# Optimization experiments

Hardware: AMD Instinct MI355X
Metric: run time of the kernel (lower is better)

The kernel has to match this reference:

```python
import jax, jax.numpy as jnp
import numpy as np
from jax import lax

FEAT_STRIDE = 16
PRE_NMS_TOP_N = 6000   # cfg['TEST'].RPN_PRE_NMS_TOP_N
POST_NMS_TOP_N = 300   # cfg['TEST'].RPN_POST_NMS_TOP_N
NMS_THRESH = 0.7       # cfg['TEST'].RPN_NMS_THRESH
MIN_SIZE = 16.0        # cfg['TEST'].RPN_MIN_SIZE
B, A, H, W = 32, 9, 128, 128
NEG_INF = jnp.float32(-1e30)


def _whctrs(a):
    w = a[2] - a[0] + 1.0
    h = a[3] - a[1] + 1.0
    return w, h, a[0] + 0.5 * (w - 1), a[1] + 0.5 * (h - 1)

def _mkanchors(ws, hs, xc, yc):
    ws = ws[:, None]; hs = hs[:, None]
    return np.hstack((xc - 0.5 * (ws - 1), yc - 0.5 * (hs - 1),
                      xc + 0.5 * (ws - 1), yc + 0.5 * (hs - 1)))

def _ratio_enum(anchor, ratios):
    w, h, xc, yc = _whctrs(anchor)
    size = w * h
    ws = np.round(np.sqrt(size / ratios))
    hs = np.round(ws * ratios)
    return _mkanchors(ws, hs, xc, yc)

def _scale_enum(anchor, scales):
    w, h, xc, yc = _whctrs(anchor)
    return _mkanchors(w * scales, h * scales, xc, yc)

def generate_anchors(base_size=16, ratios=np.array([0.5, 1.0, 2.0]), scales=np.array([8.0, 16.0, 32.0])):
    base = np.array([1, 1, base_size, base_size], dtype=np.float64) - 1
    ra = _ratio_enum(base, ratios)
    return np.vstack([_scale_enum(ra[i], scales) for i in range(ra.shape[0])]).astype(np.float32)

_BASE_ANCHORS = generate_anchors()  # (A, 4)

def _all_anchors(h, w):
    sx = np.arange(w) * FEAT_STRIDE
    sy = np.arange(h) * FEAT_STRIDE
    sx, sy = np.meshgrid(sx, sy)  # row-major (h, w) matches permute(0,2,3,1) ordering
    shifts = np.stack([sx.ravel(), sy.ravel(), sx.ravel(), sy.ravel()], axis=1).astype(np.float32)
    return jnp.asarray((shifts[:, None, :] + _BASE_ANCHORS[None, :, :]).reshape(-1, 4))  # (h*w*A, 4)

# ---- bbox_transform_inv / clip_boxes ----

def _decode(anchors, deltas):
    ws = anchors[:, 2] - anchors[:, 0] + 1.0
    hs = anchors[:, 3] - anchors[:, 1] + 1.0
    cx = anchors[:, 0] + 0.5 * ws
    cy = anchors[:, 1] + 0.5 * hs
    dx, dy, dw, dh = deltas[:, 0], deltas[:, 1], deltas[:, 2], deltas[:, 3]
    pcx = dx * ws + cx
    pcy = dy * hs + cy
    pw = jnp.exp(dw) * ws
    ph = jnp.exp(dh) * hs
    return jnp.stack([pcx - 0.5 * pw, pcy - 0.5 * ph, pcx + 0.5 * pw, pcy + 0.5 * ph], axis=1)

def _clip(b, imh, imw):
    x1 = jnp.clip(b[:, 0], 0.0, imw - 1.0)
    y1 = jnp.clip(b[:, 1], 0.0, imh - 1.0)
    x2 = jnp.clip(b[:, 2], 0.0, imw - 1.0)
    y2 = jnp.clip(b[:, 3], 0.0, imh - 1.0)
    return jnp.stack([x1, y1, x2, y2], axis=1)

# ---- greedy NMS: pick top-score box, suppress IoU > thresh, repeat POST times ----

def _nms_select(boxes, scores):
    # boxes: (PRE, 4) score-sorted; scores: (PRE,)
    areas = (boxes[:, 2] - boxes[:, 0] + 1.0) * (boxes[:, 3] - boxes[:, 1] + 1.0)

    def body(i, st):
        s, keep, valid = st
        j = jnp.argmax(s)
        keep = keep.at[i].set(j)
        valid = valid.at[i].set(s[j] > NEG_INF)
        b = boxes[j]
        xx1 = jnp.maximum(b[0], boxes[:, 0])
        yy1 = jnp.maximum(b[1], boxes[:, 1])
        xx2 = jnp.minimum(b[2], boxes[:, 2])
        yy2 = jnp.minimum(b[3], boxes[:, 3])
        inter = jnp.maximum(xx2 - xx1 + 1.0, 0.0) * jnp.maximum(yy2 - yy1 + 1.0, 0.0)
        iou = inter / jnp.maximum(areas[j] + areas - inter, 1e-6)
        s = jnp.where(iou > NMS_THRESH, NEG_INF, s)  # suppresses j itself (IoU = 1)
        return s, keep, valid

    init = (scores, jnp.zeros((POST_NMS_TOP_N,), jnp.int32), jnp.zeros((POST_NMS_TOP_N,), bool))
    _, keep, valid = lax.fori_loop(0, POST_NMS_TOP_N, body, init)
    return keep, valid

def _per_image(sc, dl, info, anchors):
    prop = _clip(_decode(anchors, dl), info[0], info[1])  # (K*A, 4)
    ws = prop[:, 2] - prop[:, 0] + 1.0
    hs = prop[:, 3] - prop[:, 1] + 1.0
    min_sz = MIN_SIZE * info[2]
    sc = jnp.where((ws >= min_sz) & (hs >= min_sz), sc, NEG_INF)
    top_s, top_i = lax.top_k(sc, PRE_NMS_TOP_N)
    cand = prop[top_i]  # (PRE, 4)
    keep, valid = _nms_select(cand, top_s)
    return cand[keep] * valid[:, None].astype(cand.dtype)  # zero-pad invalid rows

def _forward(rpn_cls_prob, rpn_bbox_pred, im_info):
    b, _, h, w = rpn_cls_prob.shape
    anchors = _all_anchors(h, w)
    scores = rpn_cls_prob[:, A:, :, :].transpose(0, 2, 3, 1).reshape(b, -1)  # (b, h*w*A)
    deltas = rpn_bbox_pred.transpose(0, 2, 3, 1).reshape(b, -1, 4)           # (b, h*w*A, 4)
    boxes = jax.vmap(lambda s, d, i: _per_image(s, d, i, anchors))(scores, deltas, im_info)
    ids = jnp.broadcast_to(jnp.arange(b, dtype=boxes.dtype)[:, None, None], (b, POST_NMS_TOP_N, 1))
    return jnp.concatenate([ids, boxes], axis=2)  # (b, POST, 5): [batch_idx, x1, y1, x2, y2]

def setup_inputs() -> dict:
    key = jax.random.key(0)
    k1, k2 = jax.random.split(key)
    rpn_cls_prob = jax.random.uniform(k1, (B, 2 * A, H, W), dtype=jnp.float32)
    rpn_bbox_pred = jax.random.normal(k2, (B, 4 * A, H, W), dtype=jnp.float32) * 0.2
    im_info = jnp.tile(jnp.array([[H * FEAT_STRIDE, W * FEAT_STRIDE, 1.0]], dtype=jnp.float32), (B, 1))
    return {"rpn_cls_prob": rpn_cls_prob, "rpn_bbox_pred": rpn_bbox_pred, "im_info": im_info}

def reference(rpn_cls_prob, rpn_bbox_pred, im_info):
    return _forward(rpn_cls_prob, rpn_bbox_pred, im_info)
```

## Files before the change

kernel.cpp:

```cpp
#include <hip/hip_runtime.h>
#include <cstdint>
#include <cstddef>

#pragma clang fp contract(off)

typedef unsigned long long u64;

#define NB 32
#define NA 9
#define NH 128
#define NW 128
#define HW (NH*NW)
#define NANCH (NA*HW)
#define PRE_N 6000
#define POST_N 300
#define CAND_CAP 8192
#define NMS_T 0.7f
#define GX_GATHER 24
#define NBOX 6144
#define CH 512

__constant__ float c_wa[9] = {184.f,368.f,736.f,128.f,256.f,512.f,88.f,176.f,352.f};
__constant__ float c_ha[9] = {96.f,192.f,384.f,128.f,256.f,512.f,176.f,352.f,704.f};

__device__ __forceinline__ float4 decode_clip(int a, int h, int w,
    float dx, float dy, float dlw, float dlh, float imh, float imw) {
  float wa = c_wa[a], ha = c_ha[a];
  float cx = (float)w * 16.0f + 8.0f;
  float cy = (float)h * 16.0f + 8.0f;
  float pcx = dx * wa + cx;
  float pcy = dy * ha + cy;
  float pw = expf(dlw) * wa;
  float ph = expf(dlh) * ha;
  float x1 = pcx - 0.5f * pw;
  float y1 = pcy - 0.5f * ph;
  float x2 = pcx + 0.5f * pw;
  float y2 = pcy + 0.5f * ph;
  float4 r;
  r.x = fminf(fmaxf(x1, 0.0f), imw - 1.0f);
  r.y = fminf(fmaxf(y1, 0.0f), imh - 1.0f);
  r.z = fminf(fmaxf(x2, 0.0f), imw - 1.0f);
  r.w = fminf(fmaxf(y2, 0.0f), imh - 1.0f);
  return r;
}

__device__ __forceinline__ unsigned score_key(float sc, float bw, float bh, float msz) {
  unsigned bits = __float_as_uint(sc);
  unsigned key = (bits & 0x80000000u) ? ~bits : (bits | 0x80000000u);
  if (!(bw >= msz && bh >= msz)) key = 0u;
  return key;
}

__device__ __forceinline__ bool sup_test4(float4 v, float ar, float4 p, float pa) {
  float xx1 = fmaxf(p.x, v.x), yy1 = fmaxf(p.y, v.y);
  float xx2 = fminf(p.z, v.z), yy2 = fminf(p.w, v.w);
  float iw = fmaxf(xx2 - xx1 + 1.0f, 0.0f);
  float ih = fmaxf(yy2 - yy1 + 1.0f, 0.0f);
  float inter = iw * ih;
  float iou = inter / fmaxf(pa + ar - inter, 1e-6f);
  return iou > NMS_T;
}

__device__ __forceinline__ u64 shfl_xor_u64(u64 x, int m) {
  int lo = __shfl_xor((int)(unsigned)x, m, 64);
  int hi = __shfl_xor((int)(unsigned)(x >> 32), m, 64);
  return ((u64)(unsigned)hi << 32) | (unsigned)lo;
}

__device__ __forceinline__ void reg_step(u64 v[8], int t, int k, int j) {
  #pragma unroll
  for (int r = 0; r < 8; ++r) {
    if ((r & j) == 0) {
      int e = (t << 3) + r;
      bool up = ((e & k) == 0);
      u64 x = v[r], y = v[r | j];
      u64 mx = x > y ? x : y, mn = x > y ? y : x;
      v[r]     = up ? mx : mn;
      v[r | j] = up ? mn : mx;
    }
  }
}

__device__ __forceinline__ void shfl_step(u64 v[8], int t, int k, int j) {
  int m = j >> 3;
  bool lower = ((t & m) == 0);
  #pragma unroll
  for (int r = 0; r < 8; ++r) {
    int e = (t << 3) + r;
    bool up = ((e & k) == 0);
    u64 pv = shfl_xor_u64(v[r], m);
    bool keepmax = (up == lower);
    u64 x = v[r];
    u64 mx = x > pv ? x : pv, mn = x > pv ? pv : x;
    v[r] = keepmax ? mx : mn;
  }
}

__device__ __forceinline__ void lds_step(u64* sm, u64 v[8], int t, int k, int j) {
  int m = j >> 3;
  __syncthreads();
  #pragma unroll
  for (int r = 0; r < 8; ++r) sm[(r << 10) | t] = v[r];
  __syncthreads();
  bool lower = ((t & m) == 0);
  bool up = (((t << 3) & k) == 0);
  bool keepmax = (up == lower);
  int pt = t ^ m;
  #pragma unroll
  for (int r = 0; r < 8; ++r) {
    u64 pv = sm[(r << 10) | pt];
    u64 x = v[r];
    u64 mx = x > pv ? x : pv, mn = x > pv ? pv : x;
    v[r] = keepmax ? mx : mn;
  }
}

__device__ void find_B(const unsigned* __restrict__ hb, unsigned* part,
                       unsigned* outB, unsigned* outCum) {
  int tid = threadIdx.x;
  unsigned s = 0;
  for (int i = 0; i < 16; ++i) s += hb[tid*16 + i];
  part[tid] = s;
  __syncthreads();
  for (int off = 1; off < 256; off <<= 1) {
    unsigned v = (tid + off < 256) ? part[tid + off] : 0u;
    __syncthreads();
    part[tid] += v;
    __syncthreads();
  }
  unsigned St = part[tid];
  unsigned Sn = (tid < 255) ? part[tid + 1] : 0u;
  if (St >= (unsigned)PRE_N && Sn < (unsigned)PRE_N) {
    unsigned cum = Sn, B = 0, cumAbove = Sn;
    for (int i = 15; i >= 0; --i) {
      unsigned v = hb[tid*16 + i];
      if (cum + v >= (unsigned)PRE_N) { B = (unsigned)(tid*16 + i); cumAbove = cum; break; }
      cum += v;
    }
    *outB = B; *outCum = cumAbove;
  }
  __syncthreads();
}

__device__ void find_thr(const unsigned* __restrict__ hb2, unsigned B, unsigned cum0,
                         unsigned* part, unsigned* outThr) {
  int tid = threadIdx.x;
  unsigned s = 0;
  for (int i = 0; i < 16; ++i) s += hb2[tid*16 + i];
  part[tid] = s;
  __syncthreads();
  for (int off = 1; off < 256; off <<= 1) {
    unsigned v = (tid + off < 256) ? part[tid + off] : 0u;
    __syncthreads();
    part[tid] += v;
    __syncthreads();
  }
  unsigned St = cum0 + part[tid];
  unsigned Sn = cum0 + ((tid < 255) ? part[tid + 1] : 0u);
  if (St >= (unsigned)PRE_N && Sn < (unsigned)PRE_N) {
    unsigned cum = Sn, t = 1u;
    for (int i = 15; i >= 0; --i) {
      unsigned v = hb2[tid*16 + i];
      if (cum + v >= (unsigned)PRE_N) {
        t = (B << 20) | ((unsigned)(tid*16 + i) << 8);
        break;
      }
      cum += v;
    }
    if (t == 0u) t = 1u;
    *outThr = t;
  }
  __syncthreads();
}

__global__ __launch_bounds__(256) void k_keys(const float* __restrict__ cls,
    const float* __restrict__ dl, const float* __restrict__ info,
    unsigned* __restrict__ keys, unsigned* __restrict__ hist) {
  __shared__ unsigned hsh[4096];
  int tid = threadIdx.x;
  for (int i = tid; i < 4096; i += 256) hsh[i] = 0;
  int t = blockIdx.x * 256 + tid;
  int b = blockIdx.y;
  int hw0 = t * 4;
  int h = hw0 >> 7;
  const float* dlb  = dl  + (size_t)b * (4*NA*HW);
  const float* clsb = cls + (size_t)b * (2*NA*HW);
  float imh = info[b*3+0], imw = info[b*3+1];
  float msz = 16.0f * info[b*3+2];
  unsigned* kb = keys + (size_t)b * NANCH;
  __syncthreads();
  #pragma unroll
  for (int a = 0; a < 9; ++a) {
    float4 dx4 = *(const float4*)&dlb[(a*4+0)*HW + hw0];
    float4 dy4 = *(const float4*)&dlb[(a*4+1)*HW + hw0];
    float4 dw4 = *(const float4*)&dlb[(a*4+2)*HW + hw0];
    float4 dh4 = *(const float4*)&dlb[(a*4+3)*HW + hw0];
    float4 sc4 = *(const float4*)&clsb[(NA+a)*HW + hw0];
    uint4 out;
    {
      float4 bx = decode_clip(a, h, (hw0+0)&127, dx4.x, dy4.x, dw4.x, dh4.x, imh, imw);
      out.x = score_key(sc4.x, bx.z-bx.x+1.0f, bx.w-bx.y+1.0f, msz);
    }
    {
      float4 bx = decode_clip(a, h, (hw0+1)&127, dx4.y, dy4.y, dw4.y, dh4.y, imh, imw);
      out.y = score_key(sc4.y, bx.z-bx.x+1.0f, bx.w-bx.y+1.0f, msz);
    }
    {
      float4 bx = decode_clip(a, h, (hw0+2)&127, dx4.z, dy4.z, dw4.z, dh4.z, imh, imw);
      out.z = score_key(sc4.z, bx.z-bx.x+1.0f, bx.w-bx.y+1.0f, msz);
    }
    {
      float4 bx = decode_clip(a, h, (hw0+3)&127, dx4.w, dy4.w, dw4.w, dh4.w, imh, imw);
      out.w = score_key(sc4.w, bx.z-bx.x+1.0f, bx.w-bx.y+1.0f, msz);
    }
    *(uint4*)&kb[a*HW + hw0] = out;
    atomicAdd(&hsh[out.x >> 20], 1u);
    atomicAdd(&hsh[out.y >> 20], 1u);
    atomicAdd(&hsh[out.z >> 20], 1u);
    atomicAdd(&hsh[out.w >> 20], 1u);
  }
  __syncthreads();
  unsigned* gb = hist + ((size_t)b << 12);
  for (int i = tid; i < 4096; i += 256) {
    unsigned v = hsh[i];
    if (v) atomicAdd(&gb[i], v);
  }
}

__global__ __launch_bounds__(256) void k_hist2(const unsigned* __restrict__ keys,
    const unsigned* __restrict__ hist1, unsigned* __restrict__ hist2) {
  __shared__ unsigned h[4096];
  __shared__ unsigned part[256];
  __shared__ unsigned sB, sCum;
  int b = blockIdx.y, tid = threadIdx.x;
  for (int i = tid; i < 4096; i += 256) h[i] = 0;
  __syncthreads();
  find_B(hist1 + ((size_t)b << 12), part, &sB, &sCum);
  unsigned B = sB;
  const unsigned* kb = keys + (size_t)b * NANCH;
  for (int i = blockIdx.x * 256 + tid; i < NANCH; i += gridDim.x * 256) {
    unsigned k = kb[i];
    if ((k >> 20) == B) atomicAdd(&h[(k >> 8) & 4095u], 1u);
  }
  __syncthreads();
  unsigned* gb = hist2 + ((size_t)b << 12);
  for (int i = tid; i < 4096; i += 256) { unsigned v = h[i]; if (v) atomicAdd(&gb[i], v); }
}

__global__ __launch_bounds__(256) void k_gather(const unsigned* __restrict__ keys,
    const unsigned* __restrict__ hist1, const unsigned* __restrict__ hist2,
    const float* __restrict__ dl, const float* __restrict__ info,
    unsigned* __restrict__ cnt, u64* __restrict__ cand,
    float4* __restrict__ boxes) {
  int b = blockIdx.y, tid = threadIdx.x;
  int lane = tid & 63, wv = tid >> 6;
  __shared__ unsigned part[256];
  __shared__ unsigned sB, sCum, sThr;
  __shared__ unsigned wcnt[4], woff[4], blkbase;
  if (tid == 0) sThr = 1u;
  __syncthreads();
  find_B(hist1 + ((size_t)b << 12), part, &sB, &sCum);
  find_thr(hist2 + ((size_t)b << 12), sB, sCum, part, &sThr);
  unsigned t_ = sThr;
  const unsigned* kb = keys + (size_t)b * NANCH;
  const float* dlb = dl + (size_t)b * (4*NA*HW);
  float imh = info[b*3+0], imw = info[b*3+1];
  u64* cb = cand + (size_t)b * CAND_CAP;
  float4* bxc = boxes + (size_t)b * CAND_CAP;
  unsigned* cp = cnt + (size_t)b * 64;
  const int PER_BLK = NANCH / GX_GATHER;
  int base0 = blockIdx.x * PER_BLK;
  for (int it = 0; it < PER_BLK / 256; ++it) {
    int j = base0 + it * 256 + tid;
    unsigned key = kb[j];
    bool pass = key >= t_;
    u64 mask = __ballot(pass);
    if (lane == 0) wcnt[wv] = (unsigned)__popcll(mask);
    __syncthreads();
    if (tid == 0) {
      unsigned s0 = 0;
      for (int w = 0; w < 4; ++w) { woff[w] = s0; s0 += wcnt[w]; }
      blkbase = s0 ? atomicAdd(cp, s0) : 0u;
    }
    __syncthreads();
    if (pass) {
      unsigned pos = blkbase + woff[wv] + (unsigned)__popcll(mask & ((1ull << lane) - 1ull));
      if (pos < CAND_CAP) {
        int a = j >> 14, hw = j & (HW - 1);
        unsigned oi = (unsigned)(hw * 9 + a);
        unsigned noi = (~oi) & 0x3FFFFu;
        cb[pos] = ((u64)key << 32) | ((u64)noi << 13) | (u64)pos;
        bxc[pos] = decode_clip(a, hw >> 7, hw & 127,
                               dlb[(a*4+0)*HW + hw], dlb[(a*4+1)*HW + hw],
                               dlb[(a*4+2)*HW + hw], dlb[(a*4+3)*HW + hw],
                               imh, imw);
      }
    }
    __syncthreads();
  }
}

__global__ __launch_bounds__(1024) void k_final4(const u64* __restrict__ cand,
    const unsigned* __restrict__ cnt, const float4* __restrict__ boxes,
    float* __restrict__ out) {
  __shared__ float4 bx[NBOX];
  __shared__ float4 cbox2[CH];
  __shared__ float  carea2[CH];
  __shared__ float4 kbox[POST_N];
  __shared__ float  karea[POST_N];
  __shared__ unsigned supf[CH];
  __shared__ u64 sup[CH][9];
  __shared__ u64 aliveM[8];
  __shared__ u64 kgW[8];
  __shared__ int s_nk;
  u64* sm = (u64*)bx;

  int b = blockIdx.x, tid = threadIdx.x;
  int lane = tid & 63;
  if (tid == 0) s_nk = 0;

  unsigned effcnt = cnt[b * 64];
  if (effcnt > CAND_CAP) effcnt = CAND_CAP;
  const u64* cb = cand + (size_t)b * CAND_CAP;
  int e0 = tid << 3;
  u64 v[8];
  #pragma unroll
  for (int r = 0; r < 8; ++r)
    v[r] = ((unsigned)(e0 + r) < effcnt) ? cb[e0 + r] : 0ull;

  for (int k = 2; k <= 8; k <<= 1)
    for (int j = k >> 1; j >= 1; j >>= 1) reg_step(v, tid, k, j);
  for (int k = 16; k <= CAND_CAP; k <<= 1) {
    int j = k >> 1;
    for (; j >= 512; j >>= 1) lds_step(sm, v, tid, k, j);
    for (; j >= 8;   j >>= 1) shfl_step(v, tid, k, j);
    for (; j >= 1;   j >>= 1) reg_step(v, tid, k, j);
  }
  __syncthreads();

  const float4* bxc = boxes + (size_t)b * CAND_CAP;
  #pragma unroll
  for (int r = 0; r < 8; ++r) {
    int rank = e0 + r;
    if (rank < NBOX) {
      u64 ck = (rank < PRE_N) ? v[r] : 0ull;
      float4 w = make_float4(0.f, 0.f, -1.f, -1.f);
      if ((unsigned)(ck >> 32) != 0u)
        w = bxc[(unsigned)(ck & 0x1FFFu)];
      bx[rank] = w;
    }
  }
  __syncthreads();

  float* ob = out + (size_t)b * (POST_N * 5);
  int c = tid & (CH - 1);
  int seg = tid >> 9;

  for (int base = 0; base < NBOX; base += CH) {
    if (tid < CH) {
      float4 w = bx[base + tid];
      supf[tid] = (w.z - w.x + 1.0f > 0.0f) ? 0u : 1u;
    }
    __syncthreads();
    int nk0 = s_nk;

    if (supf[c] == 0u && nk0 > 0) {
      float4 w = bx[base + c];
      float ar = (w.z - w.x + 1.0f) * (w.w - w.y + 1.0f);
      bool dead = false;
      for (int k = seg; k < nk0; k += 2) {
        if (sup_test4(w, ar, kbox[k], karea[k])) { dead = true; break; }
      }
      if (dead) supf[c] = 1u;
    }
    __syncthreads();

    if (tid < CH) {
      u64 am = __ballot(supf[tid] == 0u);
      if (lane == 0) aliveM[tid >> 6] = am;
    }
    __syncthreads();

    int na = 0;
    #pragma unroll
    for (int g = 0; g < 8; ++g) na += (int)__popcll(aliveM[g]);
    if (na == 0) continue;

    if (tid < CH && supf[tid] == 0u) {
      int cg2 = tid >> 6;
      int pre = 0;
      #pragma unroll
      for (int g = 0; g < 8; ++g) if (g < cg2) pre += (int)__popcll(aliveM[g]);
      pre += (int)__popcll(aliveM[cg2] & ((1ull << (tid & 63)) - 1ull));
      float4 w = bx[base + tid];
      cbox2[pre] = w;
      carea2[pre] = (w.z - w.x + 1.0f) * (w.w - w.y + 1.0f);
    }
    __syncthreads();

    {
      int i = c;
      if (i < na) {
        int ngi = (i >> 6) + 1;
        int gA = seg ? (ngi >> 1) : 0;
        int gB = seg ? ngi : (ngi >> 1);
        if (gA < gB) {
          float4 vi = cbox2[i];
          float ai = carea2[i];
          for (int g = gA; g < gB; ++g) {
            int jmax = i - (g << 6);
            if (jmax > 64) jmax = 64;
            u64 r = 0;
            #pragma unroll 4
            for (int j = 0; j < jmax; ++j) {
              if (sup_test4(vi, ai, cbox2[(g << 6) + j], carea2[(g << 6) + j]))
                r |= 1ull << j;
            }
            sup[i][g] = r;
          }
        }
      }
    }
    __syncthreads();

    if (tid < 64) {
      u64 kw[8];
      #pragma unroll
      for (int s = 0; s < 8; ++s) {
        u64 kg = 0;
        if (s * 64 < na) {
          int cc = s * 64 + lane;
          bool a = (cc < na);
          #pragma unroll
          for (int g = 0; g < 8; ++g) {
            if (g < s && a) a = (sup[cc][g] & kw[g]) == 0ull;
          }
          u64 r = a ? sup[cc][s] : 0ull;
          u64 cm = __ballot(a);
          while (cm) {
            int j = __builtin_ctzll(cm);
            kg |= 1ull << j;
            u64 rem = __ballot((r >> j) & 1ull);
            cm &= ~(rem | (1ull << j));
          }
        }
        kw[s] = kg;
      }
      if (lane == 0) {
        #pragma unroll
        for (int s = 0; s < 8; ++s) kgW[s] = kw[s];
      }
    }
    __syncthreads();

    if (tid < na) {
      int s = tid >> 6;
      u64 kgw = kgW[s];
      bool kept = (kgw >> (tid & 63)) & 1;
      int pre = 0;
      #pragma unroll
      for (int g = 0; g < 8; ++g) if (g < s) pre += (int)__popcll(kgW[g]);
      pre += (int)__popcll(kgw & ((1ull << (tid & 63)) - 1ull));
      int rank = nk0 + pre;
      if (kept && rank < POST_N) {
        float4 w = cbox2[tid];
        kbox[rank] = w; karea[rank] = carea2[tid];
        ob[rank*5+0] = (float)b;
        ob[rank*5+1] = w.x; ob[rank*5+2] = w.y; ob[rank*5+3] = w.z; ob[rank*5+4] = w.w;
      }
    }
    if (tid == 0) {
      int tot = 0;
      #pragma unroll
      for (int s = 0; s < 8; ++s) tot += (int)__popcll(kgW[s]);
      int nn = nk0 + tot;
      s_nk = nn < POST_N ? nn : POST_N;
    }
    __syncthreads();
    if (s_nk >= POST_N) break;
  }
  __syncthreads();
  int nk = s_nk;
  for (int r = nk + tid; r < POST_N; r += 1024) {
    ob[r*5+0] = (float)b;
    ob[r*5+1] = 0.f; ob[r*5+2] = 0.f; ob[r*5+3] = 0.f; ob[r*5+4] = 0.f;
  }
}

extern "C" void kernel_launch(void* const* d_in, const int* in_sizes, int n_in,
                              void* d_out, int out_size, void* d_ws, size_t ws_size,
                              hipStream_t stream) {
  const float* cls  = (const float*)d_in[0];
  const float* dl   = (const float*)d_in[1];
  const float* info = (const float*)d_in[2];
  float* out = (float*)d_out;
  char* ws = (char*)d_ws;

  const size_t OFF_KEYS = 0;
  const size_t OFF_H1   = 18874368;
  const size_t OFF_H2   = 19398656;
  const size_t OFF_CNT  = 19922944;
  const size_t OFF_CAND = 19931136;
  const size_t OFF_BOX  = 22028288;
  const size_t WS_NEED  = 26222592;
  if (ws_size < WS_NEED) return;

  unsigned* keys  = (unsigned*)(ws + OFF_KEYS);
  unsigned* h1    = (unsigned*)(ws + OFF_H1);
  unsigned* h2    = (unsigned*)(ws + OFF_H2);
  unsigned* cnt   = (unsigned*)(ws + OFF_CNT);
  u64* cand = (u64*)(ws + OFF_CAND);
  float4* boxes = (float4*)(ws + OFF_BOX);

  hipMemsetAsync(ws + OFF_H1, 0, OFF_CAND - OFF_H1, stream);

  dim3 g1(HW / 1024, NB);
  k_keys<<<g1, 256, 0, stream>>>(cls, dl, info, keys, h1);
  dim3 gh(8, NB);
  k_hist2<<<gh, 256, 0, stream>>>(keys, h1, h2);
  dim3 gg(GX_GATHER, NB);
  k_gather<<<gg, 256, 0, stream>>>(keys, h1, h2, dl, info, cnt, cand, boxes);
  k_final4<<<NB, 1024, 0, stream>>>(cand, cnt, boxes, out);
}
```

Before: 332.4 us.

## Fuse all RPN proposal stages into one cooperative kernel with grid syncs

Replaces the memset and four separate kernel launches with a single cooperative kernel of 256 blocks × 1024 threads. Grid-wide syncs separate the stages: zeroing, key/histogram build, second-level histogram, candidate gather and per-image sort+NMS. A shared-memory union lets each stage reuse the same LDS. The goal is to remove launch gaps and the memset. The trade-off is that the final sort/NMS stage now runs only on the blocks handling the 32 images, and phase 1 leaves half of each block's threads idle.

```diff
diff --git a/kernel.cpp b/kernel.cpp
--- a/kernel.cpp
+++ b/kernel.cpp
@@ -1,9 +1,11 @@
 #include <hip/hip_runtime.h>
+#include <hip/hip_cooperative_groups.h>
 #include <cstdint>
 #include <cstddef>
 
 #pragma clang fp contract(off)
 
+namespace cg = cooperative_groups;
 typedef unsigned long long u64;
 
 #define NB 32
@@ -16,9 +18,10 @@
 #define POST_N 300
 #define CAND_CAP 8192
 #define NMS_T 0.7f
-#define GX_GATHER 24
 #define NBOX 6144
 #define CH 512
+#define NBLK 256
+#define NTHR 1024
 
 __constant__ float c_wa[9] = {184.f,368.f,736.f,128.f,256.f,512.f,88.f,176.f,352.f};
 __constant__ float c_ha[9] = {96.f,192.f,384.f,128.f,256.f,512.f,176.f,352.f,704.f};
@@ -118,26 +121,31 @@
 __device__ void find_B(const unsigned* __restrict__ hb, unsigned* part,
                        unsigned* outB, unsigned* outCum) {
   int tid = threadIdx.x;
-  unsigned s = 0;
-  for (int i = 0; i < 16; ++i) s += hb[tid*16 + i];
-  part[tid] = s;
+  if (tid < 256) {
+    unsigned s = 0;
+    for (int i = 0; i < 16; ++i) s += hb[tid*16 + i];
+    part[tid] = s;
+  }
   __syncthreads();
   for (int off = 1; off < 256; off <<= 1) {
-    unsigned v = (tid + off < 256) ? part[tid + off] : 0u;
-    __syncthreads();
-    part[tid] += v;
-    __syncthreads();
-  }
-  unsigned St = part[tid];
-  unsigned Sn = (tid < 255) ? part[tid + 1] : 0u;
-  if (St >= (unsigned)PRE_N && Sn < (unsigned)PRE_N) {
-    unsigned cum = Sn, B = 0, cumAbove = Sn;
-    for (int i = 15; i >= 0; --i) {
-      unsigned v = hb[tid*16 + i];
-      if (cum + v >= (unsigned)PRE_N) { B = (unsigned)(tid*16 + i); cumAbove = cum; break; }
-      cum += v;
-    }
-    *outB = B; *outCum = cumAbove;
+    unsigned v = 0;
+    if (tid < 256 && tid + off < 256) v = part[tid + off];
+    __syncthreads();
+    if (tid < 256) part[tid] += v;
+    __syncthreads();
+  }
+  if (tid < 256) {
+    unsigned St = part[tid];
+    unsigned Sn = (tid < 255) ? part[tid + 1] : 0u;
+    if (St >= (unsigned)PRE_N && Sn < (unsigned)PRE_N) {
+      unsigned cum = Sn, B = 0, cumAbove = Sn;
+      for (int i = 15; i >= 0; --i) {
+        unsigned v = hb[tid*16 + i];
+        if (cum + v >= (unsigned)PRE_N) { B = (unsigned)(tid*16 + i); cumAbove = cum; break; }
+        cum += v;
+      }
+      *outB = B; *outCum = cumAbove;
+    }
   }
   __syncthreads();
 }
@@ -145,345 +153,390 @@
 __device__ void find_thr(const unsigned* __restrict__ hb2, unsigned B, unsigned cum0,
                          unsigned* part, unsigned* outThr) {
   int tid = threadIdx.x;
-  unsigned s = 0;
-  for (int i = 0; i < 16; ++i) s += hb2[tid*16 + i];
-  part[tid] = s;
+  if (tid < 256) {
+    unsigned s = 0;
+    for (int i = 0; i < 16; ++i) s += hb2[tid*16 + i];
+    part[tid] = s;
+  }
   __syncthreads();
   for (int off = 1; off < 256; off <<= 1) {
-    unsigned v = (tid + off < 256) ? part[tid + off] : 0u;
-    __syncthreads();
-    part[tid] += v;
-    __syncthreads();
-  }
-  unsigned St = cum0 + part[tid];
-  unsigned Sn = cum0 + ((tid < 255) ? part[tid + 1] : 0u);
-  if (St >= (unsigned)PRE_N && Sn < (unsigned)PRE_N) {
-    unsigned cum = Sn, t = 1u;
-    for (int i = 15; i >= 0; --i) {
-      unsigned v = hb2[tid*16 + i];
-      if (cum + v >= (unsigned)PRE_N) {
-        t = (B << 20) | ((unsigned)(tid*16 + i) << 8);
-        break;
-      }
-      cum += v;
-    }
-    if (t == 0u) t = 1u;
-    *outThr = t;
+    unsigned v = 0;
+    if (tid < 256 && tid + off < 256) v = part[tid + off];
+    __syncthreads();
+    if (tid < 256) part[tid] += v;
+    __syncthreads();
+  }
+  if (tid < 256) {
+    unsigned St = cum0 + part[tid];
+    unsigned Sn = cum0 + ((tid < 255) ? part[tid + 1] : 0u);
+    if (St >= (unsigned)PRE_N && Sn < (unsigned)PRE_N) {
+      unsigned cum = Sn, t = 1u;
+      for (int i = 15; i >= 0; --i) {
+        unsigned v = hb2[tid*16 + i];
+        if (cum + v >= (unsigned)PRE_N) {
+          t = (B << 20) | ((unsigned)(tid*16 + i) << 8);
+          break;
+        }
+        cum += v;
+      }
+      if (t == 0u) t = 1u;
+      *outThr = t;
+    }
   }
   __syncthreads();
 }
 
-__global__ __launch_bounds__(256) void k_keys(const float* __restrict__ cls,
-    const float* __restrict__ dl, const float* __restrict__ info,
-    unsigned* __restrict__ keys, unsigned* __restrict__ hist) {
-  __shared__ unsigned hsh[4096];
+struct P1S { unsigned hsh[4096]; };
+struct P2S { unsigned h[4096]; };
+struct P4S {
+  float4 bx[NBOX];
+  float4 cbox2[CH];
+  float  carea2[CH];
+  float4 kbox[POST_N];
+  float  karea[POST_N];
+  unsigned supf[CH];
+  u64 sup[CH][9];
+  u64 aliveM[8];
+  u64 kgW[8];
+  int s_nk;
+};
+union ShU { P1S p1; P2S p2; P4S p4; };
+
+__global__ __launch_bounds__(1024) void k_mega(
+    const float* __restrict__ cls, const float* __restrict__ dl,
+    const float* __restrict__ info, float* __restrict__ out,
+    unsigned* __restrict__ keys, unsigned* __restrict__ h1,
+    unsigned* __restrict__ h2, unsigned* __restrict__ cnt,
+    u64* __restrict__ cand, float4* __restrict__ boxes) {
+  cg::grid_group grid = cg::this_grid();
+  __shared__ ShU sh;
+  __shared__ unsigned s_part[256];
+  __shared__ unsigned s_B, s_Cum, s_Thr;
+  __shared__ unsigned s_wcnt[16], s_woff[16], s_blk;
+
   int tid = threadIdx.x;
-  for (int i = tid; i < 4096; i += 256) hsh[i] = 0;
-  int t = blockIdx.x * 256 + tid;
-  int b = blockIdx.y;
-  int hw0 = t * 4;
-  int h = hw0 >> 7;
-  const float* dlb  = dl  + (size_t)b * (4*NA*HW);
-  const float* clsb = cls + (size_t)b * (2*NA*HW);
-  float imh = info[b*3+0], imw = info[b*3+1];
-  float msz = 16.0f * info[b*3+2];
-  unsigned* kb = keys + (size_t)b * NANCH;
-  __syncthreads();
-  #pragma unroll
-  for (int a = 0; a < 9; ++a) {
-    float4 dx4 = *(const float4*)&dlb[(a*4+0)*HW + hw0];
-    float4 dy4 = *(const float4*)&dlb[(a*4+1)*HW + hw0];
-    float4 dw4 = *(const float4*)&dlb[(a*4+2)*HW + hw0];
-    float4 dh4 = *(const float4*)&dlb[(a*4+3)*HW + hw0];
-    float4 sc4 = *(const float4*)&clsb[(NA+a)*HW + hw0];
-    uint4 out;
-    {
-      float4 bx = decode_clip(a, h, (hw0+0)&127, dx4.x, dy4.x, dw4.x, dh4.x, imh, imw);
-      out.x = score_key(sc4.x, bx.z-bx.x+1.0f, bx.w-bx.y+1.0f, msz);
-    }
-    {
-      float4 bx = decode_clip(a, h, (hw0+1)&127, dx4.y, dy4.y, dw4.y, dh4.y, imh, imw);
-      out.y = score_key(sc4.y, bx.z-bx.x+1.0f, bx.w-bx.y+1.0f, msz);
-    }
-    {
-      float4 bx = decode_clip(a, h, (hw0+2)&127, dx4.z, dy4.z, dw4.z, dh4.z, imh, imw);
-      out.z = score_key(sc4.z, bx.z-bx.x+1.0f, bx.w-bx.y+1.0f, msz);
-    }
-    {
-      float4 bx = decode_clip(a, h, (hw0+3)&127, dx4.w, dy4.w, dw4.w, dh4.w, imh, imw);
-      out.w = score_key(sc4.w, bx.z-bx.x+1.0f, bx.w-bx.y+1.0f, msz);
-    }
-    *(uint4*)&kb[a*HW + hw0] = out;
-    atomicAdd(&hsh[out.x >> 20], 1u);
-    atomicAdd(&hsh[out.y >> 20], 1u);
-    atomicAdd(&hsh[out.z >> 20], 1u);
-    atomicAdd(&hsh[out.w >> 20], 1u);
-  }
-  __syncthreads();
-  unsigned* gb = hist + ((size_t)b << 12);
-  for (int i = tid; i < 4096; i += 256) {
-    unsigned v = hsh[i];
-    if (v) atomicAdd(&gb[i], v);
-  }
-}
-
-__global__ __launch_bounds__(256) void k_hist2(const unsigned* __restrict__ keys,
-    const unsigned* __restrict__ hist1, unsigned* __restrict__ hist2) {
-  __shared__ unsigned h[4096];
-  __shared__ unsigned part[256];
-  __shared__ unsigned sB, sCum;
-  int b = blockIdx.y, tid = threadIdx.x;
-  for (int i = tid; i < 4096; i += 256) h[i] = 0;
-  __syncthreads();
-  find_B(hist1 + ((size_t)b << 12), part, &sB, &sCum);
-  unsigned B = sB;
-  const unsigned* kb = keys + (size_t)b * NANCH;
-  for (int i = blockIdx.x * 256 + tid; i < NANCH; i += gridDim.x * 256) {
-    unsigned k = kb[i];
-    if ((k >> 20) == B) atomicAdd(&h[(k >> 8) & 4095u], 1u);
-  }
-  __syncthreads();
-  unsigned* gb = hist2 + ((size_t)b << 12);
-  for (int i = tid; i < 4096; i += 256) { unsigned v = h[i]; if (v) atomicAdd(&gb[i], v); }
-}
-
-__global__ __launch_bounds__(256) void k_gather(const unsigned* __restrict__ keys,
-    const unsigned* __restrict__ hist1, const unsigned* __restrict__ hist2,
-    const float* __restrict__ dl, const float* __restrict__ info,
-    unsigned* __restrict__ cnt, u64* __restrict__ cand,
-    float4* __restrict__ boxes) {
-  int b = blockIdx.y, tid = threadIdx.x;
+  int blk = blockIdx.x;
   int lane = tid & 63, wv = tid >> 6;
-  __shared__ unsigned part[256];
-  __shared__ unsigned sB, sCum, sThr;
-  __shared__ unsigned wcnt[4], woff[4], blkbase;
-  if (tid == 0) sThr = 1u;
-  __syncthreads();
-  find_B(hist1 + ((size_t)b << 12), part, &sB, &sCum);
-  find_thr(hist2 + ((size_t)b << 12), sB, sCum, part, &sThr);
-  unsigned t_ = sThr;
-  const unsigned* kb = keys + (size_t)b * NANCH;
-  const float* dlb = dl + (size_t)b * (4*NA*HW);
-  float imh = info[b*3+0], imw = info[b*3+1];
-  u64* cb = cand + (size_t)b * CAND_CAP;
-  float4* bxc = boxes + (size_t)b * CAND_CAP;
-  unsigned* cp = cnt + (size_t)b * 64;
-  const int PER_BLK = NANCH / GX_GATHER;
-  int base0 = blockIdx.x * PER_BLK;
-  for (int it = 0; it < PER_BLK / 256; ++it) {
-    int j = base0 + it * 256 + tid;
-    unsigned key = kb[j];
-    bool pass = key >= t_;
-    u64 mask = __ballot(pass);
-    if (lane == 0) wcnt[wv] = (unsigned)__popcll(mask);
-    __syncthreads();
-    if (tid == 0) {
-      unsigned s0 = 0;
-      for (int w = 0; w < 4; ++w) { woff[w] = s0; s0 += wcnt[w]; }
-      blkbase = s0 ? atomicAdd(cp, s0) : 0u;
-    }
-    __syncthreads();
-    if (pass) {
-      unsigned pos = blkbase + woff[wv] + (unsigned)__popcll(mask & ((1ull << lane) - 1ull));
-      if (pos < CAND_CAP) {
-        int a = j >> 14, hw = j & (HW - 1);
-        unsigned oi = (unsigned)(hw * 9 + a);
-        unsigned noi = (~oi) & 0x3FFFFu;
-        cb[pos] = ((u64)key << 32) | ((u64)noi << 13) | (u64)pos;
-        bxc[pos] = decode_clip(a, hw >> 7, hw & 127,
-                               dlb[(a*4+0)*HW + hw], dlb[(a*4+1)*HW + hw],
-                               dlb[(a*4+2)*HW + hw], dlb[(a*4+3)*HW + hw],
-                               imh, imw);
-      }
-    }
-    __syncthreads();
-  }
-}
-
-__global__ __launch_bounds__(1024) void k_final4(const u64* __restrict__ cand,
-    const unsigned* __restrict__ cnt, const float4* __restrict__ boxes,
-    float* __restrict__ out) {
-  __shared__ float4 bx[NBOX];
-  __shared__ float4 cbox2[CH];
-  __shared__ float  carea2[CH];
-  __shared__ float4 kbox[POST_N];
-  __shared__ float  karea[POST_N];
-  __shared__ unsigned supf[CH];
-  __shared__ u64 sup[CH][9];
-  __shared__ u64 aliveM[8];
-  __shared__ u64 kgW[8];
-  __shared__ int s_nk;
-  u64* sm = (u64*)bx;
-
-  int b = blockIdx.x, tid = threadIdx.x;
-  int lane = tid & 63;
-  if (tid == 0) s_nk = 0;
-
-  unsigned effcnt = cnt[b * 64];
-  if (effcnt > CAND_CAP) effcnt = CAND_CAP;
-  const u64* cb = cand + (size_t)b * CAND_CAP;
-  int e0 = tid << 3;
-  u64 v[8];
-  #pragma unroll
-  for (int r = 0; r < 8; ++r)
-    v[r] = ((unsigned)(e0 + r) < effcnt) ? cb[e0 + r] : 0ull;
-
-  for (int k = 2; k <= 8; k <<= 1)
-    for (int j = k >> 1; j >= 1; j >>= 1) reg_step(v, tid, k, j);
-  for (int k = 16; k <= CAND_CAP; k <<= 1) {
-    int j = k >> 1;
-    for (; j >= 512; j >>= 1) lds_step(sm, v, tid, k, j);
-    for (; j >= 8;   j >>= 1) shfl_step(v, tid, k, j);
-    for (; j >= 1;   j >>= 1) reg_step(v, tid, k, j);
-  }
-  __syncthreads();
-
-  const float4* bxc = boxes + (size_t)b * CAND_CAP;
-  #pragma unroll
-  for (int r = 0; r < 8; ++r) {
-    int rank = e0 + r;
-    if (rank < NBOX) {
-      u64 ck = (rank < PRE_N) ? v[r] : 0ull;
-      float4 w = make_float4(0.f, 0.f, -1.f, -1.f);
-      if ((unsigned)(ck >> 32) != 0u)
-        w = bxc[(unsigned)(ck & 0x1FFFu)];
-      bx[rank] = w;
-    }
-  }
-  __syncthreads();
-
-  float* ob = out + (size_t)b * (POST_N * 5);
-  int c = tid & (CH - 1);
-  int seg = tid >> 9;
-
-  for (int base = 0; base < NBOX; base += CH) {
-    if (tid < CH) {
-      float4 w = bx[base + tid];
-      supf[tid] = (w.z - w.x + 1.0f > 0.0f) ? 0u : 1u;
-    }
-    __syncthreads();
-    int nk0 = s_nk;
-
-    if (supf[c] == 0u && nk0 > 0) {
-      float4 w = bx[base + c];
-      float ar = (w.z - w.x + 1.0f) * (w.w - w.y + 1.0f);
-      bool dead = false;
-      for (int k = seg; k < nk0; k += 2) {
-        if (sup_test4(w, ar, kbox[k], karea[k])) { dead = true; break; }
-      }
-      if (dead) supf[c] = 1u;
-    }
-    __syncthreads();
-
-    if (tid < CH) {
-      u64 am = __ballot(supf[tid] == 0u);
-      if (lane == 0) aliveM[tid >> 6] = am;
-    }
-    __syncthreads();
-
-    int na = 0;
+
+  {
+    unsigned gt = (unsigned)blk * NTHR + (unsigned)tid;
+    for (unsigned i = gt; i < 264192u; i += (unsigned)NBLK * NTHR) h1[i] = 0u;
+  }
+  grid.sync();
+
+  {
+    int b = blk >> 3;
+    for (int i = tid; i < 4096; i += NTHR) sh.p1.hsh[i] = 0u;
+    __syncthreads();
+    float imh = info[b*3+0], imw = info[b*3+1];
+    float msz = 16.0f * info[b*3+2];
+    if (tid < 512) {
+      int t = ((blk & 7) << 9) + tid;
+      int hw0 = t * 4;
+      int h = hw0 >> 7;
+      const float* dlb  = dl  + (size_t)b * (4*NA*HW);
+      const float* clsb = cls + (size_t)b * (2*NA*HW);
+      unsigned* kb = keys + (size_t)b * NANCH;
+      #pragma unroll
+      for (int a = 0; a < 9; ++a) {
+        float4 dx4 = *(const float4*)&dlb[(a*4+0)*HW + hw0];
+        float4 dy4 = *(const float4*)&dlb[(a*4+1)*HW + hw0];
+        float4 dw4 = *(const float4*)&dlb[(a*4+2)*HW + hw0];
+        float4 dh4 = *(const float4*)&dlb[(a*4+3)*HW + hw0];
+        float4 sc4 = *(const float4*)&clsb[(NA+a)*HW + hw0];
+        uint4 o;
+        { float4 bb = decode_clip(a, h, (hw0+0)&127, dx4.x, dy4.x, dw4.x, dh4.x, imh, imw);
+          o.x = score_key(sc4.x, bb.z-bb.x+1.0f, bb.w-bb.y+1.0f, msz); }
+        { float4 bb = decode_clip(a, h, (hw0+1)&127, dx4.y, dy4.y, dw4.y, dh4.y, imh, imw);
+          o.y = score_key(sc4.y, bb.z-bb.x+1.0f, bb.w-bb.y+1.0f, msz); }
+        { float4 bb = decode_clip(a, h, (hw0+2)&127, dx4.z, dy4.z, dw4.z, dh4.z, imh, imw);
+          o.z = score_key(sc4.z, bb.z-bb.x+1.0f, bb.w-bb.y+1.0f, msz); }
+        { float4 bb = decode_clip(a, h, (hw0+3)&127, dx4.w, dy4.w, dw4.w, dh4.w, imh, imw);
+          o.w = score_key(sc4.w, bb.z-bb.x+1.0f, bb.w-bb.y+1.0f, msz); }
+        *(uint4*)&kb[a*HW + hw0] = o;
+        atomicAdd(&sh.p1.hsh[o.x >> 20], 1u);
+        atomicAdd(&sh.p1.hsh[o.y >> 20], 1u);
+        atomicAdd(&sh.p1.hsh[o.z >> 20], 1u);
+        atomicAdd(&sh.p1.hsh[o.w >> 20], 1u);
+      }
+    }
+    __syncthreads();
+    unsigned* gb = h1 + ((size_t)(blk >> 3) << 12);
+    for (int i = tid; i < 4096; i += NTHR) {
+      unsigned v = sh.p1.hsh[i];
+      if (v) atomicAdd(&gb[i], v);
+    }
+  }
+  grid.sync();
+
+  {
+    int b = blk >> 3;
+    for (int i = tid; i < 4096; i += NTHR) sh.p2.h[i] = 0u;
+    __syncthreads();
+    find_B(h1 + ((size_t)b << 12), s_part, &s_B, &s_Cum);
+    unsigned B = s_B;
+    const uint4* kb4 = (const uint4*)(keys + (size_t)b * NANCH);
+    int p = ((blk & 7) << 10) + tid;
+    for (int i = p; i < NANCH/4; i += 8 * NTHR) {
+      uint4 kk = kb4[i];
+      if ((kk.x >> 20) == B) atomicAdd(&sh.p2.h[(kk.x >> 8) & 4095u], 1u);
+      if ((kk.y >> 20) == B) atomicAdd(&sh.p2.h[(kk.y >> 8) & 4095u], 1u);
+      if ((kk.z >> 20) == B) atomicAdd(&sh.p2.h[(kk.z >> 8) & 4095u], 1u);
+      if ((kk.w >> 20) == B) atomicAdd(&sh.p2.h[(kk.w >> 8) & 4095u], 1u);
+    }
+    __syncthreads();
+    unsigned* gb = h2 + ((size_t)b << 12);
+    for (int i = tid; i < 4096; i += NTHR) {
+      unsigned v = sh.p2.h[i];
+      if (v) atomicAdd(&gb[i], v);
+    }
+  }
+  grid.sync();
+
+  {
+    int b = blk >> 3;
+    if (tid == 0) s_Thr = 1u;
+    __syncthreads();
+    find_B(h1 + ((size_t)b << 12), s_part, &s_B, &s_Cum);
+    find_thr(h2 + ((size_t)b << 12), s_B, s_Cum, s_part, &s_Thr);
+    unsigned t_ = s_Thr;
+    const unsigned* kb = keys + (size_t)b * NANCH;
+    const float* dlb = dl + (size_t)b * (4*NA*HW);
+    float imh = info[b*3+0], imw = info[b*3+1];
+    u64* cb = cand + (size_t)b * CAND_CAP;
+    float4* bxc = boxes + (size_t)b * CAND_CAP;
+    unsigned* cp = cnt + (size_t)b * 64;
+    int base0 = (blk & 7) * (NANCH / 8);
+    for (int it = 0; it < 9; ++it) {
+      int j0 = base0 + it * 2048 + tid * 2;
+      uint2 kk = *(const uint2*)&kb[j0];
+      bool p0 = kk.x >= t_, p1 = kk.y >= t_;
+      u64 m0 = __ballot(p0), m1 = __ballot(p1);
+      unsigned tot = (unsigned)(__popcll(m0) + __popcll(m1));
+      if (lane == 0) s_wcnt[wv] = tot;
+      __syncthreads();
+      if (tid == 0) {
+        unsigned s0 = 0;
+        for (int w = 0; w < 16; ++w) { s_woff[w] = s0; s0 += s_wcnt[w]; }
+        s_blk = s0 ? atomicAdd(cp, s0) : 0u;
+      }
+      __syncthreads();
+      u64 lt = (1ull << lane) - 1ull;
+      unsigned wb = s_blk + s_woff[wv];
+      if (p0) {
+        unsigned pos = wb + (unsigned)__popcll(m0 & lt);
+        if (pos < CAND_CAP) {
+          int j = j0;
+          int a = j >> 14, hw = j & (HW - 1);
+          unsigned oi = (unsigned)(hw * 9 + a);
+          unsigned noi = (~oi) & 0x3FFFFu;
+          cb[pos] = ((u64)kk.x << 32) | ((u64)noi << 13) | (u64)pos;
+          bxc[pos] = decode_clip(a, hw >> 7, hw & 127,
+                                 dlb[(a*4+0)*HW + hw], dlb[(a*4+1)*HW + hw],
+                                 dlb[(a*4+2)*HW + hw], dlb[(a*4+3)*HW + hw],
+                                 imh, imw);
+        }
+      }
+      if (p1) {
+        unsigned pos = wb + (unsigned)__popcll(m0) + (unsigned)__popcll(m1 & lt);
+        if (pos < CAND_CAP) {
+          int j = j0 + 1;
+          int a = j >> 14, hw = j & (HW - 1);
+          unsigned oi = (unsigned)(hw * 9 + a);
+          unsigned noi = (~oi) & 0x3FFFFu;
+          cb[pos] = ((u64)kk.y << 32) | ((u64)noi << 13) | (u64)pos;
+          bxc[pos] = decode_clip(a, hw >> 7, hw & 127,
+                                 dlb[(a*4+0)*HW + hw], dlb[(a*4+1)*HW + hw],
+                                 dlb[(a*4+2)*HW + hw], dlb[(a*4+3)*HW + hw],
+                                 imh, imw);
+        }
+      }
+    }
+  }
+  grid.sync();
+
+  if (blk >= NB) return;
+  {
+    int b = blk;
+    u64* sm = (u64*)sh.p4.bx;
+    float4* bx = sh.p4.bx;
+    float4* cbox2 = sh.p4.cbox2;
+    float*  carea2 = sh.p4.carea2;
+    float4* kbox = sh.p4.kbox;
+    float*  karea = sh.p4.karea;
+    unsigned* supf = sh.p4.supf;
+    u64 (*sup)[9] = sh.p4.sup;
+    u64* aliveM = sh.p4.aliveM;
+    u64* kgW = sh.p4.kgW;
+
+    if (tid == 0) sh.p4.s_nk = 0;
+
+    unsigned effcnt = cnt[b * 64];
+    if (effcnt > CAND_CAP) effcnt = CAND_CAP;
+    const u64* cb = cand + (size_t)b * CAND_CAP;
+    int e0 = tid << 3;
+    u64 v[8];
     #pragma unroll
-    for (int g = 0; g < 8; ++g) na += (int)__popcll(aliveM[g]);
-    if (na == 0) continue;
-
-    if (tid < CH && supf[tid] == 0u) {
-      int cg2 = tid >> 6;
-      int pre = 0;
+    for (int r = 0; r < 8; ++r)
+      v[r] = ((unsigned)(e0 + r) < effcnt) ? cb[e0 + r] : 0ull;
+
+    for (int k = 2; k <= 8; k <<= 1)
+      for (int j = k >> 1; j >= 1; j >>= 1) reg_step(v, tid, k, j);
+    for (int k = 16; k <= CAND_CAP; k <<= 1) {
+      int j = k >> 1;
+      for (; j >= 512; j >>= 1) lds_step(sm, v, tid, k, j);
+      for (; j >= 8;   j >>= 1) shfl_step(v, tid, k, j);
+      for (; j >= 1;   j >>= 1) reg_step(v, tid, k, j);
+    }
+    __syncthreads();
+
+    const float4* bxc = boxes + (size_t)b * CAND_CAP;
+    #pragma unroll
+    for (int r = 0; r < 8; ++r) {
+      int rank = e0 + r;
+      if (rank < NBOX) {
+        u64 ck = (rank < PRE_N) ? v[r] : 0ull;
+        float4 w = make_float4(0.f, 0.f, -1.f, -1.f);
+        if ((unsigned)(ck >> 32) != 0u)
+          w = bxc[(unsigned)(ck & 0x1FFFu)];
+        bx[rank] = w;
+      }
+    }
+    __syncthreads();
+
+    float* ob = out + (size_t)b * (POST_N * 5);
+    int c = tid & (CH - 1);
+    int seg = tid >> 9;
+
+    for (int base = 0; base < NBOX; base += CH) {
+      if (tid < CH) {
+        float4 w = bx[base + tid];
+        supf[tid] = (w.z - w.x + 1.0f > 0.0f) ? 0u : 1u;
+      }
+      __syncthreads();
+      int nk0 = sh.p4.s_nk;
+
+      if (supf[c] == 0u && nk0 > 0) {
+        float4 w = bx[base + c];
+        float ar = (w.z - w.x + 1.0f) * (w.w - w.y + 1.0f);
+        bool dead = false;
+        for (int k = seg; k < nk0; k += 2) {
+          if (sup_test4(w, ar, kbox[k], karea[k])) { dead = true; break; }
+        }
+        if (dead) supf[c] = 1u;
+      }
+      __syncthreads();
+
+      if (tid < CH) {
+        u64 am = __ballot(supf[tid] == 0u);
+        if (lane == 0) aliveM[tid >> 6] = am;
+      }
+      __syncthreads();
+
+      int na = 0;
       #pragma unroll
-      for (int g = 0; g < 8; ++g) if (g < cg2) pre += (int)__popcll(aliveM[g]);
-      pre += (int)__popcll(aliveM[cg2] & ((1ull << (tid & 63)) - 1ull));
-      float4 w = bx[base + tid];
-      cbox2[pre] = w;
-      carea2[pre] = (w.z - w.x + 1.0f) * (w.w - w.y + 1.0f);
-    }
-    __syncthreads();
-
-    {
-      int i = c;
-      if (i < na) {
-        int ngi = (i >> 6) + 1;
-        int gA = seg ? (ngi >> 1) : 0;
-        int gB = seg ? ngi : (ngi >> 1);
-        if (gA < gB) {
-          float4 vi = cbox2[i];
-          float ai = carea2[i];
-          for (int g = gA; g < gB; ++g) {
-            int jmax = i - (g << 6);
-            if (jmax > 64) jmax = 64;
-            u64 r = 0;
-            #pragma unroll 4
-            for (int j = 0; j < jmax; ++j) {
-              if (sup_test4(vi, ai, cbox2[(g << 6) + j], carea2[(g << 6) + j]))
-                r |= 1ull << j;
+      for (int g = 0; g < 8; ++g) na += (int)__popcll(aliveM[g]);
+      if (na == 0) continue;
+
+      if (tid < CH && supf[tid] == 0u) {
+        int cg2 = tid >> 6;
+        int pre = 0;
+        #pragma unroll
+        for (int g = 0; g < 8; ++g) if (g < cg2) pre += (int)__popcll(aliveM[g]);
+        pre += (int)__popcll(aliveM[cg2] & ((1ull << (tid & 63)) - 1ull));
+        float4 w = bx[base + tid];
+        cbox2[pre] = w;
+        carea2[pre] = (w.z - w.x + 1.0f) * (w.w - w.y + 1.0f);
+      }
+      __syncthreads();
+
+      {
+        int i = c;
+        if (i < na) {
+          int ngi = (i >> 6) + 1;
+          int gA = seg ? (ngi >> 1) : 0;
+          int gB = seg ? ngi : (ngi >> 1);
+          if (gA < gB) {
+            float4 vi = cbox2[i];
+            float ai = carea2[i];
+            for (int g = gA; g < gB; ++g) {
+              int jmax = i - (g << 6);
+              if (jmax > 64) jmax = 64;
+              u64 r = 0;
+              #pragma unroll 4
+              for (int j = 0; j < jmax; ++j) {
+                if (sup_test4(vi, ai, cbox2[(g << 6) + j], carea2[(g << 6) + j]))
+                  r |= 1ull << j;
+              }
+              sup[i][g] = r;
             }
-            sup[i][g] = r;
           }
         }
       }
-    }
-    __syncthreads();
-
-    if (tid < 64) {
-      u64 kw[8];
-      #pragma unroll
-      for (int s = 0; s < 8; ++s) {
-        u64 kg = 0;
-        if (s * 64 < na) {
-          int cc = s * 64 + lane;
-          bool a = (cc < na);
+      __syncthreads();
+
+      if (tid < 64) {
+        u64 kw[8];
+        #pragma unroll
+        for (int s = 0; s < 8; ++s) {
+          u64 kg = 0;
+          if (s * 64 < na) {
+            int cc = s * 64 + lane;
+            bool a = (cc < na);
+            #pragma unroll
+            for (int g = 0; g < 8; ++g) {
+              if (g < s && a) a = (sup[cc][g] & kw[g]) == 0ull;
+            }
+            u64 r = a ? sup[cc][s] : 0ull;
+            u64 cm = __ballot(a);
+            while (cm) {
+              int j = __builtin_ctzll(cm);
+              kg |= 1ull << j;
+              u64 rem = __ballot((r >> j) & 1ull);
+              cm &= ~(rem | (1ull << j));
+            }
+          }
+          kw[s] = kg;
+        }
+        if (lane == 0) {
           #pragma unroll
-          for (int g = 0; g < 8; ++g) {
-            if (g < s && a) a = (sup[cc][g] & kw[g]) == 0ull;
-          }
-          u64 r = a ? sup[cc][s] : 0ull;
-          u64 cm = __ballot(a);
-          while (cm) {
-            int j = __builtin_ctzll(cm);
-            kg |= 1ull << j;
-            u64 rem = __ballot((r >> j) & 1ull);
-            cm &= ~(rem | (1ull << j));
-          }
-        }
-        kw[s] = kg;
-      }
-      if (lane == 0) {
+          for (int s = 0; s < 8; ++s) kgW[s] = kw[s];
+        }
+      }
+      __syncthreads();
+
+      if (tid < na) {
+        int s = tid >> 6;
+        u64 kgw = kgW[s];
+        bool kept = (kgw >> (tid & 63)) & 1;
+        int pre = 0;
         #pragma unroll
-        for (int s = 0; s < 8; ++s) kgW[s] = kw[s];
-      }
-    }
-    __syncthreads();
-
-    if (tid < na) {
-      int s = tid >> 6;
-      u64 kgw = kgW[s];
-      bool kept = (kgw >> (tid & 63)) & 1;
-      int pre = 0;
-      #pragma unroll
-      for (int g = 0; g < 8; ++g) if (g < s) pre += (int)__popcll(kgW[g]);
-      pre += (int)__popcll(kgw & ((1ull << (tid & 63)) - 1ull));
-      int rank = nk0 + pre;
-      if (kept && rank < POST_N) {
-        float4 w = cbox2[tid];
-        kbox[rank] = w; karea[rank] = carea2[tid];
-        ob[rank*5+0] = (float)b;
-        ob[rank*5+1] = w.x; ob[rank*5+2] = w.y; ob[rank*5+3] = w.z; ob[rank*5+4] = w.w;
-      }
-    }
-    if (tid == 0) {
-      int tot = 0;
-      #pragma unroll
-      for (int s = 0; s < 8; ++s) tot += (int)__popcll(kgW[s]);
-      int nn = nk0 + tot;
-      s_nk = nn < POST_N ? nn : POST_N;
-    }
-    __syncthreads();
-    if (s_nk >= POST_N) break;
-  }
-  __syncthreads();
-  int nk = s_nk;
-  for (int r = nk + tid; r < POST_N; r += 1024) {
-    ob[r*5+0] = (float)b;
-    ob[r*5+1] = 0.f; ob[r*5+2] = 0.f; ob[r*5+3] = 0.f; ob[r*5+4] = 0.f;
+        for (int g = 0; g < 8; ++g) if (g < s) pre += (int)__popcll(kgW[g]);
+        pre += (int)__popcll(kgw & ((1ull << (tid & 63)) - 1ull));
+        int rank = nk0 + pre;
+        if (kept && rank < POST_N) {
+          float4 w = cbox2[tid];
+          kbox[rank] = w; karea[rank] = carea2[tid];
+          ob[rank*5+0] = (float)b;
+          ob[rank*5+1] = w.x; ob[rank*5+2] = w.y; ob[rank*5+3] = w.z; ob[rank*5+4] = w.w;
+        }
+      }
+      if (tid == 0) {
+        int tot = 0;
+        #pragma unroll
+        for (int s = 0; s < 8; ++s) tot += (int)__popcll(kgW[s]);
+        int nn = nk0 + tot;
+        sh.p4.s_nk = nn < POST_N ? nn : POST_N;
+      }
+      __syncthreads();
+      if (sh.p4.s_nk >= POST_N) break;
+    }
+    __syncthreads();
+    int nk = sh.p4.s_nk;
+    for (int r = nk + tid; r < POST_N; r += NTHR) {
+      ob[r*5+0] = (float)b;
+      ob[r*5+1] = 0.f; ob[r*5+2] = 0.f; ob[r*5+3] = 0.f; ob[r*5+4] = 0.f;
+    }
   }
 }
 
@@ -512,13 +565,9 @@
   u64* cand = (u64*)(ws + OFF_CAND);
   float4* boxes = (float4*)(ws + OFF_BOX);
 
-  hipMemsetAsync(ws + OFF_H1, 0, OFF_CAND - OFF_H1, stream);
-
-  dim3 g1(HW / 1024, NB);
-  k_keys<<<g1, 256, 0, stream>>>(cls, dl, info, keys, h1);
-  dim3 gh(8, NB);
-  k_hist2<<<gh, 256, 0, stream>>>(keys, h1, h2);
-  dim3 gg(GX_GATHER, NB);
-  k_gather<<<gg, 256, 0, stream>>>(keys, h1, h2, dl, info, cnt, cand, boxes);
-  k_final4<<<NB, 1024, 0, stream>>>(cand, cnt, boxes, out);
-}
+  void* kargs[] = { (void*)&cls, (void*)&dl, (void*)&info, (void*)&out,
+                    (void*)&keys, (void*)&h1, (void*)&h2, (void*)&cnt,
+                    (void*)&cand, (void*)&boxes };
+  hipLaunchCooperativeKernel(reinterpret_cast<void*>(k_mega),
+                             dim3(NBLK), dim3(NTHR), kargs, 0, stream);
+}
```

Result: slower. 416.7 us (+25.4%).
